# Kernel tuning notes

Measured on AMD Instinct MI355X. Metric: run time of the kernel, lower is better.

Reference implementation:

```python
import jax, jax.numpy as jnp
import numpy as np

B, T, D, H = 4, 2048, 384, 6
HD = D // H  # 64
HALF = HD // 2


def setup_inputs() -> dict:
    key = jax.random.key(0)
    k0, k1, k2 = jax.random.split(key, 3)
    x = jax.random.normal(k0, (B, T, D), jnp.float32)
    attn_bias = jnp.zeros((1, 1, T, T), jnp.float32)  # additive SDPA bias
    # standard RoPE tables: [T, HD/2]
    inv_freq = 1.0 / (10000.0 ** (np.arange(HALF, dtype=np.float32) / HALF))
    ang = np.arange(T, dtype=np.float32)[:, None] * inv_freq[None, :]
    cos = jnp.asarray(np.cos(ang), jnp.float32)
    sin = jnp.asarray(np.sin(ang), jnp.float32)
    w_qkv = jax.random.normal(k1, (D, 3 * D), jnp.float32) * (D ** -0.5)
    w_proj = jax.random.normal(k2, (D, D), jnp.float32) * (D ** -0.5)
    return {"x": x, "attn_bias": attn_bias, "cos": cos, "sin": sin,
            "w_qkv": w_qkv, "w_proj": w_proj}


def _apply_rope(x, cos, sin):
    # x: [b, h, t, hd]; cos/sin: [t, hd/2] -> rotate-half RoPE
    half = x.shape[-1] // 2
    x1, x2 = x[..., :half], x[..., half:]
    c = cos[None, None, :, :]
    s = sin[None, None, :, :]
    return jnp.concatenate([x1 * c - x2 * s, x2 * c + x1 * s], axis=-1)


def reference(x, attn_bias, cos, sin, w_qkv, w_proj):
    b, t, _ = x.shape
    qkv = (x @ w_qkv).reshape(b, t, 3, H, HD)  # fused QKV projection
    q = jnp.transpose(qkv[:, :, 0], (0, 2, 1, 3))  # [b,h,t,hd]
    k = jnp.transpose(qkv[:, :, 1], (0, 2, 1, 3))
    v = jnp.transpose(qkv[:, :, 2], (0, 2, 1, 3))
    q = _apply_rope(q, cos, sin)
    k = _apply_rope(k, cos, sin)
    scale = 1.0 / jnp.sqrt(jnp.asarray(HD, x.dtype))
    scores = jnp.einsum("bhqd,bhkd->bhqk", q, k) * scale + attn_bias
    attn = jax.nn.softmax(scores, axis=-1)
    out = jnp.einsum("bhqk,bhkd->bhqd", attn, v)
    out = jnp.transpose(out, (0, 2, 1, 3)).reshape(b, t, H * HD)
    return out @ w_proj
```

## Files before the change

kernel.cpp:

```cpp
#include <hip/hip_runtime.h>
#include <hip/hip_bf16.h>

#define BB   4
#define TT   2048
#define DDIM 384
#define HH   6
#define HD   64
#define BT   (BB*TT)
#define QKVC (3*DDIM)

#define QSCALE 0.18033688011112042f
#define LOG2E  1.4426950408889634f

typedef __attribute__((ext_vector_type(4))) short short4v;
typedef __attribute__((ext_vector_type(8))) short short8v;
typedef __attribute__((ext_vector_type(4))) float float4v;
typedef unsigned short u16;

static __device__ __forceinline__ u16 f2bu(float f) {
    __hip_bfloat16 h = __float2bfloat16(f);
    return __builtin_bit_cast(u16, h);
}
static __device__ __forceinline__ unsigned pk2(float lo, float hi) {
    return (unsigned)f2bu(lo) | ((unsigned)f2bu(hi) << 16);
}
static __device__ __forceinline__ short8v frag4(uint4 v) {
    return __builtin_bit_cast(short8v, v);
}
static __device__ __forceinline__ short8v ld_frag(const u16* p) {
    short4v a = *(const short4v*)p;
    short4v b = *(const short4v*)(p + 4);
    return __builtin_shufflevector(a, b, 0, 1, 2, 3, 4, 5, 6, 7);
}
static __device__ __forceinline__ void st8(u16* p, uint4 v) {
    *(uint2*)p       = make_uint2(v.x, v.y);
    *(uint2*)(p + 4) = make_uint2(v.z, v.w);
}
static __device__ __forceinline__ void pl32swap(unsigned &a, unsigned &b) {
    auto r = __builtin_amdgcn_permlane32_swap(a, b, false, false);
    a = r[0]; b = r[1];
}
static __device__ __forceinline__ void pl16swap(unsigned &a, unsigned &b) {
    auto r = __builtin_amdgcn_permlane16_swap(a, b, false, false);
    a = r[0]; b = r[1];
}

#define MFMA16(a, b, c) __builtin_amdgcn_mfma_f32_16x16x32_bf16((a), (b), (c), 0, 0, 0)

__global__ __launch_bounds__(256) void prep_kernel(
    const float* __restrict__ wqkv, const float* __restrict__ wproj,
    const float* __restrict__ x, const float* __restrict__ bias,
    u16* __restrict__ wqkvT, u16* __restrict__ wprojT,
    u16* __restrict__ xb, unsigned* __restrict__ flag)
{
    const int bid = blockIdx.x;
    const int t = threadIdx.x;
    if (bid >= 912) {
        const float* gp = bias + (size_t)(bid - 912) * 4096 + (size_t)t * 16;
        unsigned acc = 0;
        #pragma unroll
        for (int u = 0; u < 4; ++u) {
            float4 v = *(const float4*)(gp + 4 * u);
            acc |= (__builtin_bit_cast(unsigned, v.x) & 0x7fffffffu);
            acc |= (__builtin_bit_cast(unsigned, v.y) & 0x7fffffffu);
            acc |= (__builtin_bit_cast(unsigned, v.z) & 0x7fffffffu);
            acc |= (__builtin_bit_cast(unsigned, v.w) & 0x7fffffffu);
        }
        if (acc) atomicOr(flag, 1u);
        return;
    }
    if (bid >= 144) {
        size_t base = (size_t)(bid - 144) * 4096 + (size_t)t * 16;
        const float* gp = x + base;
        __align__(16) u16 tmp[16];
        #pragma unroll
        for (int u = 0; u < 4; ++u) {
            float4 v = *(const float4*)(gp + 4 * u);
            tmp[4 * u + 0] = f2bu(v.x); tmp[4 * u + 1] = f2bu(v.y);
            tmp[4 * u + 2] = f2bu(v.z); tmp[4 * u + 3] = f2bu(v.w);
        }
        *(uint4*)(xb + base)     = *(const uint4*)tmp;
        *(uint4*)(xb + base + 8) = *(const uint4*)(tmp + 8);
        return;
    }
    const float* in; u16* out; int K, C, c0, k0;
    if (bid < 108) { in = wqkv;  out = wqkvT;  K = DDIM; C = QKVC;
                     c0 = (bid % 18) * 64; k0 = (bid / 18) * 64; }
    else           { int b2 = bid - 108; in = wproj; out = wprojT; K = DDIM; C = DDIM;
                     c0 = (b2 % 6) * 64; k0 = (b2 / 6) * 64; }
    __shared__ float tr[64][65];
    {
        int kr = t >> 2, cb = (t & 3) * 16;
        const float* gp = in + (size_t)(k0 + kr) * C + c0 + cb;
        #pragma unroll
        for (int u = 0; u < 4; ++u) {
            float4 v = *(const float4*)(gp + 4 * u);
            tr[cb + 4 * u + 0][kr] = v.x;
            tr[cb + 4 * u + 1][kr] = v.y;
            tr[cb + 4 * u + 2][kr] = v.z;
            tr[cb + 4 * u + 3][kr] = v.w;
        }
    }
    __syncthreads();
    {
        int c = t >> 2, kb = (t & 3) * 16;
        __align__(16) u16 tmp[16];
        #pragma unroll
        for (int u = 0; u < 16; ++u) tmp[u] = f2bu(tr[c][kb + u]);
        u16* op = out + (size_t)(c0 + c) * K + k0 + kb;
        *(uint4*)op       = *(const uint4*)tmp;
        *(uint4*)(op + 8) = *(const uint4*)(tmp + 8);
    }
}

__global__ __launch_bounds__(256, 4) void qkv_rope_kernel(
    const u16* __restrict__ xb, const u16* __restrict__ wt,
    const float* __restrict__ cs, const float* __restrict__ sn,
    u16* __restrict__ qb, u16* __restrict__ kb, u16* __restrict__ vtb)
{
    __shared__ __align__(16) u16 xs[2][64][68];
    __shared__ __align__(16) u16 ws[2][64][68];
    const int t = threadIdx.x;
    const int wv = t >> 6, lane = t & 63, quad = lane >> 4, lo = lane & 15;
    const int r0 = blockIdx.y * 64;
    const int c0 = blockIdx.x * 64;
    const int sr = t >> 3, sd = (t & 7) * 8;

    st8(&xs[0][sr][sd],      *(const uint4*)(xb + (size_t)(r0 + sr) * DDIM + sd));
    st8(&xs[0][sr + 32][sd], *(const uint4*)(xb + (size_t)(r0 + sr + 32) * DDIM + sd));
    st8(&ws[0][sr][sd],      *(const uint4*)(wt + (size_t)(c0 + sr) * DDIM + sd));
    st8(&ws[0][sr + 32][sd], *(const uint4*)(wt + (size_t)(c0 + sr + 32) * DDIM + sd));
    __syncthreads();

    float4v acc[4] = {};
    for (int kk = 0; kk < 6; ++kk) {
        const int cur = kk & 1, nxt = cur ^ 1;
        const int kkn = (kk < 5 ? kk + 1 : 5) * 64;
        uint4 xp0 = *(const uint4*)(xb + (size_t)(r0 + sr) * DDIM + kkn + sd);
        uint4 xp1 = *(const uint4*)(xb + (size_t)(r0 + sr + 32) * DDIM + kkn + sd);
        uint4 wp0 = *(const uint4*)(wt + (size_t)(c0 + sr) * DDIM + kkn + sd);
        uint4 wp1 = *(const uint4*)(wt + (size_t)(c0 + sr + 32) * DDIM + kkn + sd);

        #pragma unroll
        for (int kf = 0; kf < 2; ++kf) {
            short8v a = ld_frag(&xs[cur][16 * wv + lo][kf * 32 + quad * 8]);
            #pragma unroll
            for (int nt = 0; nt < 4; ++nt) {
                short8v b = ld_frag(&ws[cur][nt * 16 + lo][kf * 32 + quad * 8]);
                acc[nt] = MFMA16(a, b, acc[nt]);
            }
        }
        st8(&xs[nxt][sr][sd], xp0);
        st8(&xs[nxt][sr + 32][sd], xp1);
        st8(&ws[nxt][sr][sd], wp0);
        st8(&ws[nxt][sr + 32][sd], wp1);
        __syncthreads();
    }

    const int sec = blockIdx.x / 6;
    const int h   = blockIdx.x % 6;
    const int rbase = r0 + 16 * wv + 4 * quad;
    const int bidx  = r0 >> 11;
    const int tbase = rbase & (TT - 1);

    if (sec == 2) {
        #pragma unroll
        for (int nt = 0; nt < 4; ++nt) {
            int d = nt * 16 + lo;
            unsigned a0 = pk2(acc[nt][0], acc[nt][1]);
            unsigned a1 = pk2(acc[nt][2], acc[nt][3]);
            u16* gp = vtb + ((size_t)(bidx * HH + h) * HD + d) * TT + tbase;
            *(uint2*)gp = make_uint2(a0, a1);
        }
    } else {
        u16* dst = (sec == 0) ? qb : kb;
        const float scl = (sec == 0) ? QSCALE : 1.0f;
        #pragma unroll
        for (int np = 0; np < 2; ++np) {
            #pragma unroll
            for (int r = 0; r < 4; ++r) {
                int tpos = tbase + r;
                int ci = np * 16 + lo;
                float cv = cs[tpos * 32 + ci];
                float sv = sn[tpos * 32 + ci];
                float x1 = acc[np][r], x2 = acc[np + 2][r];
                u16* gp = dst + ((size_t)(bidx * HH + h) * TT + tpos) * HD;
                gp[ci]      = f2bu((x1 * cv - x2 * sv) * scl);
                gp[ci + 32] = f2bu((x2 * cv + x1 * sv) * scl);
            }
        }
    }
}

__global__ __launch_bounds__(256, 2) void attn_ksplit_kernel(
    const u16* __restrict__ qb, const u16* __restrict__ kb, const u16* __restrict__ vtb,
    const unsigned* __restrict__ flag, u16* __restrict__ ob)
{
    if (*flag != 0u) return;

    __shared__ __align__(16) float red_o[2][64][68];
    __shared__ float red_l[4][64];

    const int t = threadIdx.x;
    const int wv = t >> 6, lane = t & 63, quad = lane >> 4, lo = lane & 15;
    const int bh = blockIdx.x;
    const int b = bh / HH, h = bh % HH;
    const int q0 = blockIdx.y * 64;

    short8v aq[4][2];
    #pragma unroll
    for (int g = 0; g < 4; ++g) {
        const u16* qp = qb + ((size_t)bh * TT + q0 + g * 16 + lo) * HD + quad * 8;
        aq[g][0] = frag4(*(const uint4*)qp);
        aq[g][1] = frag4(*(const uint4*)(qp + 32));
    }

    const u16* kbase = kb + ((size_t)bh * TT + lo) * HD + quad * 8;
    const u16* vbase = vtb + ((size_t)bh * HD + lo) * TT + quad * 8;

    uint4 kq[4][2], vq[4][2];
    {
        const size_t ko = (size_t)wv * 64 * HD;
        const size_t vo = (size_t)wv * 64;
        #pragma unroll
        for (int nt = 0; nt < 4; ++nt) {
            kq[nt][0] = *(const uint4*)(kbase + ko + (size_t)nt * 16 * HD);
            kq[nt][1] = *(const uint4*)(kbase + ko + (size_t)nt * 16 * HD + 32);
        }
        #pragma unroll
        for (int dt = 0; dt < 4; ++dt) {
            vq[dt][0] = *(const uint4*)(vbase + (size_t)dt * 16 * TT + vo);
            vq[dt][1] = *(const uint4*)(vbase + (size_t)dt * 16 * TT + vo + 32);
        }
    }

    float4v oacc[4][4] = {};
    float lacc[4] = {0.f, 0.f, 0.f, 0.f};

    for (int j = 0; j < 8; ++j) {
        const int ktn = (j < 7) ? (wv + 4 * (j + 1)) : wv;
        const size_t kno = (size_t)ktn * 64 * HD;
        const size_t vno = (size_t)ktn * 64;

        #pragma unroll
        for (int g = 0; g < 4; ++g) {
            float4v s[4] = {};
            #pragma unroll
            for (int nt = 0; nt < 4; ++nt)
                s[nt] = MFMA16(frag4(kq[nt][0]), aq[g][0], s[nt]);
            #pragma unroll
            for (int nt = 0; nt < 4; ++nt)
                s[nt] = MFMA16(frag4(kq[nt][1]), aq[g][1], s[nt]);
            if (g == 3) {
                #pragma unroll
                for (int nt = 0; nt < 4; ++nt) {
                    kq[nt][0] = *(const uint4*)(kbase + kno + (size_t)nt * 16 * HD);
                    kq[nt][1] = *(const uint4*)(kbase + kno + (size_t)nt * 16 * HD + 32);
                }
            }

            unsigned w[8];
            #pragma unroll
            for (int nt = 0; nt < 4; ++nt) {
                float p0 = __builtin_amdgcn_exp2f(s[nt][0]);
                float p1 = __builtin_amdgcn_exp2f(s[nt][1]);
                float p2 = __builtin_amdgcn_exp2f(s[nt][2]);
                float p3 = __builtin_amdgcn_exp2f(s[nt][3]);
                lacc[g] += (p0 + p1) + (p2 + p3);
                w[2 * nt]     = pk2(p0, p1);
                w[2 * nt + 1] = pk2(p2, p3);
            }

            pl32swap(w[0], w[2]); pl16swap(w[0], w[2]);
            pl32swap(w[1], w[3]); pl16swap(w[1], w[3]);
            pl32swap(w[4], w[6]); pl16swap(w[4], w[6]);
            pl32swap(w[5], w[7]); pl16swap(w[5], w[7]);
            short8v pa0 = frag4(make_uint4(w[0], w[1], w[2], w[3]));
            short8v pa1 = frag4(make_uint4(w[4], w[5], w[6], w[7]));

            #pragma unroll
            for (int dt = 0; dt < 4; ++dt)
                oacc[g][dt] = MFMA16(pa0, frag4(vq[dt][0]), oacc[g][dt]);
            #pragma unroll
            for (int dt = 0; dt < 4; ++dt)
                oacc[g][dt] = MFMA16(pa1, frag4(vq[dt][1]), oacc[g][dt]);
            if (g == 3) {
                #pragma unroll
                for (int dt = 0; dt < 4; ++dt) {
                    vq[dt][0] = *(const uint4*)(vbase + (size_t)dt * 16 * TT + vno);
                    vq[dt][1] = *(const uint4*)(vbase + (size_t)dt * 16 * TT + vno + 32);
                }
            }
        }
    }

    #pragma unroll
    for (int g = 0; g < 4; ++g) {
        lacc[g] += __shfl_xor(lacc[g], 16);
        lacc[g] += __shfl_xor(lacc[g], 32);
    }
    if (quad == 0) {
        #pragma unroll
        for (int g = 0; g < 4; ++g) red_l[wv][g * 16 + lo] = lacc[g];
    }
    float* slot0 = &red_o[0][0][0] + (size_t)lane * 68;
    float* slot1 = &red_o[1][0][0] + (size_t)lane * 68;
    if (wv == 1 || wv == 3) {
        float* sp = (wv == 1) ? slot0 : slot1;
        #pragma unroll
        for (int g = 0; g < 4; ++g)
            #pragma unroll
            for (int dt = 0; dt < 4; ++dt)
                *(float4v*)(sp + (g * 4 + dt) * 4) = oacc[g][dt];
    }
    __syncthreads();
    if (wv == 0 || wv == 2) {
        float* sp = (wv == 0) ? slot0 : slot1;
        #pragma unroll
        for (int g = 0; g < 4; ++g)
            #pragma unroll
            for (int dt = 0; dt < 4; ++dt)
                oacc[g][dt] += *(const float4v*)(sp + (g * 4 + dt) * 4);
    }
    __syncthreads();
    if (wv == 2) {
        #pragma unroll
        for (int g = 0; g < 4; ++g)
            #pragma unroll
            for (int dt = 0; dt < 4; ++dt)
                *(float4v*)(slot1 + (g * 4 + dt) * 4) = oacc[g][dt];
    }
    __syncthreads();
    if (wv == 0) {
        #pragma unroll
        for (int g = 0; g < 4; ++g) {
            #pragma unroll
            for (int dt = 0; dt < 4; ++dt)
                oacc[g][dt] += *(const float4v*)(slot1 + (g * 4 + dt) * 4);
            float lt = red_l[0][g * 16 + lo] + red_l[1][g * 16 + lo]
                     + red_l[2][g * 16 + lo] + red_l[3][g * 16 + lo];
            #pragma unroll
            for (int r = 0; r < 4; ++r) {
                float lr = __shfl(lt, 4 * quad + r);
                float inv = 1.f / lr;
                u16* gp = ob + ((size_t)b * TT + q0 + g * 16 + 4 * quad + r) * DDIM
                             + h * HD + lo;
                #pragma unroll
                for (int dt = 0; dt < 4; ++dt)
                    gp[dt * 16] = f2bu(oacc[g][dt][r] * inv);
            }
        }
    }
}

__global__ __launch_bounds__(256, 4) void attn_bias_kernel(
    const u16* __restrict__ qb, const u16* __restrict__ kb, const u16* __restrict__ vtb,
    const float* __restrict__ bias, const unsigned* __restrict__ flag,
    u16* __restrict__ ob)
{
    if (*flag == 0u) return;

    __shared__ __align__(16) u16 ks[2][64][68];
    __shared__ __align__(16) u16 vt[2][64][68];

    const int t = threadIdx.x;
    const int wv = t >> 6, lane = t & 63, quad = lane >> 4, lo = lane & 15;
    const int bh = blockIdx.x;
    const int b = bh / HH, h = bh % HH;
    const int q0 = blockIdx.y * 64;
    const int qrow = q0 + 16 * wv + lo;

    const u16* qbase = qb + ((size_t)bh * TT + qrow) * HD + quad * 8;
    short8v aq0 = frag4(*(const uint4*)qbase);
    short8v aq1 = frag4(*(const uint4*)(qbase + 32));

    const int sr = t >> 3, sd = (t & 7) * 8;
    const u16* kbbase = kb + (size_t)bh * TT * HD;
    const u16* vtbase = vtb + (size_t)bh * HD * TT;
    const float* brow = bias + (size_t)qrow * TT + 4 * quad;

    st8(&ks[0][sr][sd],      *(const uint4*)(kbbase + (size_t)sr * HD + sd));
    st8(&ks[0][sr + 32][sd], *(const uint4*)(kbbase + (size_t)(sr + 32) * HD + sd));
    st8(&vt[0][sr][sd],      *(const uint4*)(vtbase + (size_t)sr * TT + sd));
    st8(&vt[0][sr + 32][sd], *(const uint4*)(vtbase + (size_t)(sr + 32) * TT + sd));
    float4 bcur[4];
    #pragma unroll
    for (int nt = 0; nt < 4; ++nt) bcur[nt] = *(const float4*)(brow + nt * 16);
    __syncthreads();

    float4v oacc[4] = {};
    float lacc[4] = {0.f, 0.f, 0.f, 0.f};

    for (int kt = 0; kt < TT / 64; ++kt) {
        const int cur = kt & 1, nxt = cur ^ 1;
        const int kn = (kt < 31 ? kt + 1 : 31) * 64;

        uint4 kp0 = *(const uint4*)(kbbase + (size_t)(kn + sr) * HD + sd);
        uint4 kp1 = *(const uint4*)(kbbase + (size_t)(kn + sr + 32) * HD + sd);
        uint4 vp0 = *(const uint4*)(vtbase + (size_t)sr * TT + kn + sd);
        uint4 vp1 = *(const uint4*)(vtbase + (size_t)(sr + 32) * TT + kn + sd);
        float4 bnxt[4];
        #pragma unroll
        for (int nt = 0; nt < 4; ++nt) bnxt[nt] = *(const float4*)(brow + kn + nt * 16);

        float4v s[4] = {};
        #pragma unroll
        for (int kf = 0; kf < 2; ++kf) {
            #pragma unroll
            for (int nt = 0; nt < 4; ++nt) {
                short8v kfr = ld_frag(&ks[cur][nt * 16 + lo][kf * 32 + quad * 8]);
                s[nt] = MFMA16(kfr, (kf ? aq1 : aq0), s[nt]);
            }
        }

        unsigned w[8];
        #pragma unroll
        for (int nt = 0; nt < 4; ++nt) {
            float p0 = __builtin_amdgcn_exp2f(fmaf(bcur[nt].x, LOG2E, s[nt][0]));
            float p1 = __builtin_amdgcn_exp2f(fmaf(bcur[nt].y, LOG2E, s[nt][1]));
            float p2 = __builtin_amdgcn_exp2f(fmaf(bcur[nt].z, LOG2E, s[nt][2]));
            float p3 = __builtin_amdgcn_exp2f(fmaf(bcur[nt].w, LOG2E, s[nt][3]));
            lacc[nt] += (p0 + p1) + (p2 + p3);
            w[2 * nt]     = pk2(p0, p1);
            w[2 * nt + 1] = pk2(p2, p3);
        }

        pl32swap(w[0], w[2]); pl16swap(w[0], w[2]);
        pl32swap(w[1], w[3]); pl16swap(w[1], w[3]);
        pl32swap(w[4], w[6]); pl16swap(w[4], w[6]);
        pl32swap(w[5], w[7]); pl16swap(w[5], w[7]);
        short8v pa0 = frag4(make_uint4(w[0], w[1], w[2], w[3]));
        short8v pa1 = frag4(make_uint4(w[4], w[5], w[6], w[7]));

        #pragma unroll
        for (int kf = 0; kf < 2; ++kf) {
            #pragma unroll
            for (int dt = 0; dt < 4; ++dt) {
                short8v bv = ld_frag(&vt[cur][dt * 16 + lo][kf * 32 + quad * 8]);
                oacc[dt] = MFMA16((kf ? pa1 : pa0), bv, oacc[dt]);
            }
        }

        st8(&ks[nxt][sr][sd], kp0);
        st8(&ks[nxt][sr + 32][sd], kp1);
        st8(&vt[nxt][sr][sd], vp0);
        st8(&vt[nxt][sr + 32][sd], vp1);
        #pragma unroll
        for (int nt = 0; nt < 4; ++nt) bcur[nt] = bnxt[nt];
        __syncthreads();
    }

    float l = (lacc[0] + lacc[1]) + (lacc[2] + lacc[3]);
    l += __shfl_xor(l, 16);
    l += __shfl_xor(l, 32);
    #pragma unroll
    for (int r = 0; r < 4; ++r) {
        float lr = __shfl(l, 4 * quad + r);
        float inv = 1.f / lr;
        u16* gp = ob + ((size_t)b * TT + q0 + 16 * wv + 4 * quad + r) * DDIM + h * HD + lo;
        #pragma unroll
        for (int dt = 0; dt < 4; ++dt)
            gp[dt * 16] = f2bu(oacc[dt][r] * inv);
    }
}

__global__ __launch_bounds__(256, 4) void proj_kernel(
    const u16* __restrict__ o, const u16* __restrict__ wt, float* __restrict__ out)
{
    __shared__ __align__(16) u16 os[2][64][68];
    __shared__ __align__(16) u16 ws[2][64][68];
    const int t = threadIdx.x;
    const int wv = t >> 6, lane = t & 63, quad = lane >> 4, lo = lane & 15;
    const int r0 = blockIdx.y * 64, c0 = blockIdx.x * 64;
    const int sr = t >> 3, sd = (t & 7) * 8;

    st8(&os[0][sr][sd],      *(const uint4*)(o + (size_t)(r0 + sr) * DDIM + sd));
    st8(&os[0][sr + 32][sd], *(const uint4*)(o + (size_t)(r0 + sr + 32) * DDIM + sd));
    st8(&ws[0][sr][sd],      *(const uint4*)(wt + (size_t)(c0 + sr) * DDIM + sd));
    st8(&ws[0][sr + 32][sd], *(const uint4*)(wt + (size_t)(c0 + sr + 32) * DDIM + sd));
    __syncthreads();

    float4v acc[4] = {};
    for (int kk = 0; kk < 6; ++kk) {
        const int cur = kk & 1, nxt = cur ^ 1;
        const int kkn = (kk < 5 ? kk + 1 : 5) * 64;
        uint4 op0 = *(const uint4*)(o + (size_t)(r0 + sr) * DDIM + kkn + sd);
        uint4 op1 = *(const uint4*)(o + (size_t)(r0 + sr + 32) * DDIM + kkn + sd);
        uint4 wp0 = *(const uint4*)(wt + (size_t)(c0 + sr) * DDIM + kkn + sd);
        uint4 wp1 = *(const uint4*)(wt + (size_t)(c0 + sr + 32) * DDIM + kkn + sd);

        #pragma unroll
        for (int kf = 0; kf < 2; ++kf) {
            short8v a = ld_frag(&os[cur][16 * wv + lo][kf * 32 + quad * 8]);
            #pragma unroll
            for (int nt = 0; nt < 4; ++nt) {
                short8v bfr = ld_frag(&ws[cur][nt * 16 + lo][kf * 32 + quad * 8]);
                acc[nt] = MFMA16(a, bfr, acc[nt]);
            }
        }
        st8(&os[nxt][sr][sd], op0);
        st8(&os[nxt][sr + 32][sd], op1);
        st8(&ws[nxt][sr][sd], wp0);
        st8(&ws[nxt][sr + 32][sd], wp1);
        __syncthreads();
    }
    #pragma unroll
    for (int r = 0; r < 4; ++r) {
        float* gp = out + (size_t)(r0 + 16 * wv + 4 * quad + r) * DDIM + c0;
        #pragma unroll
        for (int nt = 0; nt < 4; ++nt)
            gp[nt * 16 + lo] = acc[nt][r];
    }
}

extern "C" void kernel_launch(void* const* d_in, const int* in_sizes, int n_in,
                              void* d_out, int out_size, void* d_ws, size_t ws_size,
                              hipStream_t stream) {
    const float* x     = (const float*)d_in[0];
    const float* bias  = (const float*)d_in[1];
    const float* cs    = (const float*)d_in[2];
    const float* sn    = (const float*)d_in[3];
    const float* wqkv  = (const float*)d_in[4];
    const float* wproj = (const float*)d_in[5];
    float* out = (float*)d_out;

    u16* wqkvT  = (u16*)d_ws;
    u16* wprojT = wqkvT + (size_t)QKVC * DDIM;
    u16* qb     = wprojT + (size_t)DDIM * DDIM;
    u16* kb     = qb + (size_t)BB * HH * TT * HD;
    u16* vtb    = kb + (size_t)BB * HH * TT * HD;
    u16* ob     = vtb + (size_t)BB * HH * TT * HD;
    u16* xb     = ob + (size_t)BT * DDIM;
    unsigned* flag = (unsigned*)(xb + (size_t)BT * DDIM);

    hipMemsetAsync(flag, 0, sizeof(unsigned), stream);
    prep_kernel<<<dim3(144 + BT * DDIM / 4096 + TT * TT / 4096), 256, 0, stream>>>(
        wqkv, wproj, x, bias, wqkvT, wprojT, xb, flag);
    qkv_rope_kernel<<<dim3(QKVC / 64, BT / 64), 256, 0, stream>>>(
        xb, wqkvT, cs, sn, qb, kb, vtb);
    attn_ksplit_kernel<<<dim3(BB * HH, TT / 64), 256, 0, stream>>>(
        qb, kb, vtb, flag, ob);
    attn_bias_kernel<<<dim3(BB * HH, TT / 64), 256, 0, stream>>>(
        qb, kb, vtb, bias, flag, ob);
    proj_kernel<<<dim3(DDIM / 64, BT / 64), 256, 0, stream>>>(ob, wprojT, out);
}
```

Before: 167.3 us.

## Stage full-K weight tile in LDS and load A fragments directly into registers

The QKV and output-projection GEMMs no longer double-buffer 64-wide K chunks with a barrier per step. Each block now loads its whole 64x384 weight tile into LDS once, and each wave loads its A-operand fragments straight from global memory into registers. This leaves a single barrier and an unrolled 12-step MFMA loop. The cost is more LDS per block (about 50KB) and more registers, so launch bounds drop to 3 blocks per CU.

Result: slower. 171.7 us (+2.6%).

```diff
diff --git a/kernel.cpp b/kernel.cpp
--- a/kernel.cpp
+++ b/kernel.cpp
@@ -113,48 +113,42 @@
     }
 }
 
-__global__ __launch_bounds__(256, 4) void qkv_rope_kernel(
+__global__ __launch_bounds__(256, 3) void qkv_rope_kernel(
     const u16* __restrict__ xb, const u16* __restrict__ wt,
     const float* __restrict__ cs, const float* __restrict__ sn,
     u16* __restrict__ qb, u16* __restrict__ kb, u16* __restrict__ vtb)
 {
-    __shared__ __align__(16) u16 xs[2][64][68];
-    __shared__ __align__(16) u16 ws[2][64][68];
+    __shared__ __align__(16) u16 ws[64][392];
     const int t = threadIdx.x;
     const int wv = t >> 6, lane = t & 63, quad = lane >> 4, lo = lane & 15;
-    const int r0 = blockIdx.y * 64;
-    const int c0 = blockIdx.x * 64;
-    const int sr = t >> 3, sd = (t & 7) * 8;
-
-    st8(&xs[0][sr][sd],      *(const uint4*)(xb + (size_t)(r0 + sr) * DDIM + sd));
-    st8(&xs[0][sr + 32][sd], *(const uint4*)(xb + (size_t)(r0 + sr + 32) * DDIM + sd));
-    st8(&ws[0][sr][sd],      *(const uint4*)(wt + (size_t)(c0 + sr) * DDIM + sd));
-    st8(&ws[0][sr + 32][sd], *(const uint4*)(wt + (size_t)(c0 + sr + 32) * DDIM + sd));
+    const int r0 = blockIdx.y * 64, c0 = blockIdx.x * 64;
+
+    {
+        const uint4* src = (const uint4*)(wt + (size_t)c0 * DDIM);
+        #pragma unroll
+        for (int u = 0; u < 12; ++u) {
+            int idx = t + u * 256;
+            int f = idx * 8;
+            int row = f / DDIM, col = f % DDIM;
+            *(uint4*)&ws[row][col] = src[idx];
+        }
+    }
+    const u16* arow = xb + (size_t)(r0 + 16 * wv + lo) * DDIM + quad * 8;
+    uint4 af[12];
+    #pragma unroll
+    for (int kf = 0; kf < 12; ++kf)
+        af[kf] = *(const uint4*)(arow + kf * 32);
     __syncthreads();
 
     float4v acc[4] = {};
-    for (int kk = 0; kk < 6; ++kk) {
-        const int cur = kk & 1, nxt = cur ^ 1;
-        const int kkn = (kk < 5 ? kk + 1 : 5) * 64;
-        uint4 xp0 = *(const uint4*)(xb + (size_t)(r0 + sr) * DDIM + kkn + sd);
-        uint4 xp1 = *(const uint4*)(xb + (size_t)(r0 + sr + 32) * DDIM + kkn + sd);
-        uint4 wp0 = *(const uint4*)(wt + (size_t)(c0 + sr) * DDIM + kkn + sd);
-        uint4 wp1 = *(const uint4*)(wt + (size_t)(c0 + sr + 32) * DDIM + kkn + sd);
-
-        #pragma unroll
-        for (int kf = 0; kf < 2; ++kf) {
-            short8v a = ld_frag(&xs[cur][16 * wv + lo][kf * 32 + quad * 8]);
-            #pragma unroll
-            for (int nt = 0; nt < 4; ++nt) {
-                short8v b = ld_frag(&ws[cur][nt * 16 + lo][kf * 32 + quad * 8]);
-                acc[nt] = MFMA16(a, b, acc[nt]);
-            }
-        }
-        st8(&xs[nxt][sr][sd], xp0);
-        st8(&xs[nxt][sr + 32][sd], xp1);
-        st8(&ws[nxt][sr][sd], wp0);
-        st8(&ws[nxt][sr + 32][sd], wp1);
-        __syncthreads();
+    #pragma unroll
+    for (int kf = 0; kf < 12; ++kf) {
+        short8v a = frag4(af[kf]);
+        #pragma unroll
+        for (int nt = 0; nt < 4; ++nt) {
+            short8v b = ld_frag(&ws[nt * 16 + lo][kf * 32 + quad * 8]);
+            acc[nt] = MFMA16(a, b, acc[nt]);
+        }
     }
 
     const int sec = blockIdx.x / 6;
@@ -464,45 +458,40 @@
     }
 }
 
-__global__ __launch_bounds__(256, 4) void proj_kernel(
+__global__ __launch_bounds__(256, 3) void proj_kernel(
     const u16* __restrict__ o, const u16* __restrict__ wt, float* __restrict__ out)
 {
-    __shared__ __align__(16) u16 os[2][64][68];
-    __shared__ __align__(16) u16 ws[2][64][68];
+    __shared__ __align__(16) u16 ws[64][392];
     const int t = threadIdx.x;
     const int wv = t >> 6, lane = t & 63, quad = lane >> 4, lo = lane & 15;
     const int r0 = blockIdx.y * 64, c0 = blockIdx.x * 64;
-    const int sr = t >> 3, sd = (t & 7) * 8;
-
-    st8(&os[0][sr][sd],      *(const uint4*)(o + (size_t)(r0 + sr) * DDIM + sd));
-    st8(&os[0][sr + 32][sd], *(const uint4*)(o + (size_t)(r0 + sr + 32) * DDIM + sd));
-    st8(&ws[0][sr][sd],      *(const uint4*)(wt + (size_t)(c0 + sr) * DDIM + sd));
-    st8(&ws[0][sr + 32][sd], *(const uint4*)(wt + (size_t)(c0 + sr + 32) * DDIM + sd));
+
+    {
+        const uint4* src = (const uint4*)(wt + (size_t)c0 * DDIM);
+        #pragma unroll
+        for (int u = 0; u < 12; ++u) {
+            int idx = t + u * 256;
+            int f = idx * 8;
+            int row = f / DDIM, col = f % DDIM;
+            *(uint4*)&ws[row][col] = src[idx];
+        }
+    }
+    const u16* arow = o + (size_t)(r0 + 16 * wv + lo) * DDIM + quad * 8;
+    uint4 af[12];
+    #pragma unroll
+    for (int kf = 0; kf < 12; ++kf)
+        af[kf] = *(const uint4*)(arow + kf * 32);
     __syncthreads();
 
     float4v acc[4] = {};
-    for (int kk = 0; kk < 6; ++kk) {
-        const int cur = kk & 1, nxt = cur ^ 1;
-        const int kkn = (kk < 5 ? kk + 1 : 5) * 64;
-        uint4 op0 = *(const uint4*)(o + (size_t)(r0 + sr) * DDIM + kkn + sd);
-        uint4 op1 = *(const uint4*)(o + (size_t)(r0 + sr + 32) * DDIM + kkn + sd);
-        uint4 wp0 = *(const uint4*)(wt + (size_t)(c0 + sr) * DDIM + kkn + sd);
-        uint4 wp1 = *(const uint4*)(wt + (size_t)(c0 + sr + 32) * DDIM + kkn + sd);
-
-        #pragma unroll
-        for (int kf = 0; kf < 2; ++kf) {
-            short8v a = ld_frag(&os[cur][16 * wv + lo][kf * 32 + quad * 8]);
-            #pragma unroll
-            for (int nt = 0; nt < 4; ++nt) {
-                short8v bfr = ld_frag(&ws[cur][nt * 16 + lo][kf * 32 + quad * 8]);
-                acc[nt] = MFMA16(a, bfr, acc[nt]);
-            }
-        }
-        st8(&os[nxt][sr][sd], op0);
-        st8(&os[nxt][sr + 32][sd], op1);
-        st8(&ws[nxt][sr][sd], wp0);
-        st8(&ws[nxt][sr + 32][sd], wp1);
-        __syncthreads();
+    #pragma unroll
+    for (int kf = 0; kf < 12; ++kf) {
+        short8v a = frag4(af[kf]);
+        #pragma unroll
+        for (int nt = 0; nt < 4; ++nt) {
+            short8v b = ld_frag(&ws[nt * 16 + lo][kf * 32 + quad * 8]);
+            acc[nt] = MFMA16(a, b, acc[nt]);
+        }
     }
     #pragma unroll
     for (int r = 0; r < 4; ++r) {
```
